# Kernel optimization log

Measured on AMD Instinct MI355X. Metric: run time of the kernel, lower is better.

The kernel has to match this reference:

```python
import jax, jax.numpy as jnp
import numpy as np
from jax import lax

VOCAB = 32000; D = 1024; NL = 4; DI = 2048; S = 16; R = 64; DC = 4
B = 1; L = 1024; EPS = 1e-5


def setup_inputs() -> dict:
    key = jax.random.key(0)
    ks = jax.random.split(key, 16)
    def n(k, shape, s=0.02):
        return jax.random.normal(k, shape, dtype=jnp.float32) * s
    return dict(
        tokens=jax.random.randint(ks[0], (B, L), 0, VOCAB),
        embed=n(ks[1], (VOCAB, D)),
        norm_w=jnp.ones((NL, D), jnp.float32) + n(ks[2], (NL, D)),
        in_proj_w=n(ks[3], (NL, 2 * DI, D)),
        conv_w=n(ks[4], (NL, DI, DC), 0.1),
        conv_b=n(ks[5], (NL, DI)),
        x_proj_w=n(ks[6], (NL, R + 2 * S, DI)),
        dt_proj_w=n(ks[7], (NL, DI, R), 0.1),
        dt_proj_b=n(ks[8], (NL, DI), 0.5),
        A_log=n(ks[9], (NL, DI, S), 0.5),
        D_param=jnp.ones((NL, DI), jnp.float32) + n(ks[10], (NL, DI)),
        out_proj_w=n(ks[11], (NL, D, DI)),
        norm_f_w=jnp.ones((D,), jnp.float32),
        lm_head_w=n(ks[12], (VOCAB, D)),
    )


def _rmsnorm(x, w):
    return x * lax.rsqrt(jnp.mean(x * x, axis=-1, keepdims=True) + EPS) * w


def _mamba_block(x, norm_w, in_w, cw, cb, xw, dtw, dtb, a_log, dp, ow):
    # x: [B, L, D]
    res = x
    x = _rmsnorm(x, norm_w)
    xz = jnp.einsum('bld,ed->ble', x, in_w)      # [B, L, 2*DI]
    u, z = xz[..., :DI], xz[..., DI:]
    # depthwise causal conv over time
    u = jnp.swapaxes(u, 1, 2)                    # [B, DI, L]
    u = lax.conv_general_dilated(u, cw[:, None, :], (1,), [(DC - 1, 0)],
                                 feature_group_count=DI,
                                 dimension_numbers=('NCH', 'OIH', 'NCH'))
    u = jax.nn.silu(u + cb[None, :, None])
    u = jnp.swapaxes(u, 1, 2)                    # [B, L, DI]
    # input-dependent SSM params
    dbc = jnp.einsum('bld,ed->ble', u, xw)       # [B, L, R+2S]
    dt = jax.nn.softplus(jnp.einsum('blr,dr->bld', dbc[..., :R], dtw) + dtb)
    Bm = dbc[..., R:R + S]                       # [B, L, S]
    Cm = dbc[..., R + S:]                        # [B, L, S]
    A = -jnp.exp(a_log)                          # [DI, S]
    dA = jnp.exp(dt[..., None] * A)              # [B, L, DI, S]
    dBu = (dt * u)[..., None] * Bm[:, :, None, :]  # [B, L, DI, S]
    # selective scan over time
    def step(h, inp):
        a_t, b_t, c_t = inp
        h = a_t * h + b_t                        # [B, DI, S]
        y = jnp.einsum('bds,bs->bd', h, c_t)
        return h, y
    h0 = jnp.zeros((x.shape[0], DI, S), x.dtype)
    _, ys = lax.scan(step, h0, (jnp.moveaxis(dA, 1, 0), jnp.moveaxis(dBu, 1, 0), jnp.moveaxis(Cm, 1, 0)))
    y = jnp.moveaxis(ys, 0, 1) + u * dp          # [B, L, DI]
    y = y * jax.nn.silu(z)
    return res + jnp.einsum('bld,od->blo', y, ow)


def reference(tokens, embed, norm_w, in_proj_w, conv_w, conv_b, x_proj_w,
              dt_proj_w, dt_proj_b, A_log, D_param, out_proj_w, norm_f_w, lm_head_w):
    x = embed[tokens]                            # [B, L, D]
    for i in range(NL):
        x = _mamba_block(x, norm_w[i], in_proj_w[i], conv_w[i], conv_b[i],
                         x_proj_w[i], dt_proj_w[i], dt_proj_b[i], A_log[i],
                         D_param[i], out_proj_w[i])
    x = _rmsnorm(x, norm_f_w)
    return jnp.einsum('bld,vd->blv', x, lm_head_w)  # [B, L, VOCAB]
```

## Files before the change

### kernel.cpp

```cpp
#include <hip/hip_runtime.h>
#include <hip/hip_bf16.h>
#include <math.h>


typedef __attribute__((ext_vector_type(8))) short bf16x8;
typedef __attribute__((ext_vector_type(4))) float f32x4;

__device__ __forceinline__ short f2bf(float f) {
  union { float f; unsigned u; } v; v.f = f;
  unsigned u = v.u;
  unsigned r = (u + 0x7FFFu + ((u >> 16) & 1u)) >> 16;
  return (short)r;
}

__device__ __forceinline__ bf16x8 pack8(float4 a, float4 b) {
  bf16x8 r;
  r[0] = f2bf(a.x); r[1] = f2bf(a.y); r[2] = f2bf(a.z); r[3] = f2bf(a.w);
  r[4] = f2bf(b.x); r[5] = f2bf(b.y); r[6] = f2bf(b.z); r[7] = f2bf(b.w);
  return r;
}

__device__ __forceinline__ float softplus_f(float x) {
  return (x > 20.f) ? x : log1pf(__expf(x));
}

__device__ __forceinline__ void gl_lds16(const void* g, void* l) {
  void* gnc = (void*)g;
  __builtin_amdgcn_global_load_lds((__attribute__((address_space(1))) void*)gnc,
                                   (__attribute__((address_space(3))) void*)l, 16, 0, 0);
}

__global__ __launch_bounds__(256) void cvt_all_k(const float* __restrict__ s0, unsigned short* __restrict__ d0, int n0,
                                                 const float* __restrict__ s1, unsigned short* __restrict__ d1, int n1,
                                                 const float* __restrict__ s2, unsigned short* __restrict__ d2, int n2,
                                                 const float* __restrict__ s3, unsigned short* __restrict__ d3, int n3,
                                                 const float* __restrict__ s4, unsigned short* __restrict__ d4, int n4) {
  int stride = gridDim.x * 256;
  int tot = n0 + n1 + n2 + n3 + n4;
  for (int i = blockIdx.x * 256 + threadIdx.x; i < tot; i += stride) {
    const float* s; unsigned short* d; int j = i;
    if (j < n0) { s = s0; d = d0; }
    else { j -= n0; if (j < n1) { s = s1; d = d1; }
      else { j -= n1; if (j < n2) { s = s2; d = d2; }
        else { j -= n2; if (j < n3) { s = s3; d = d3; }
          else { j -= n3; s = s4; d = d4; } } } }
    const float4* p = (const float4*)(s + (size_t)j * 8);
    float4 a = p[0], b = p[1];
    *(bf16x8*)(d + (size_t)j * 8) = pack8(a, b);
  }
}

__global__ __launch_bounds__(256) void embed_rms_k(const int* __restrict__ tok,
                                                   const float* __restrict__ emb,
                                                   const float* __restrict__ w,
                                                   float* __restrict__ x,
                                                   unsigned short* __restrict__ xn16) {
  int l = blockIdx.x;
  int t = tok[l];
  float4 v = ((const float4*)(emb + (size_t)t * 1024))[threadIdx.x];
  ((float4*)(x + (size_t)l * 1024))[threadIdx.x] = v;
  float ss = v.x * v.x + v.y * v.y + v.z * v.z + v.w * v.w;
  ss += __shfl_down(ss, 32); ss += __shfl_down(ss, 16); ss += __shfl_down(ss, 8);
  ss += __shfl_down(ss, 4);  ss += __shfl_down(ss, 2);  ss += __shfl_down(ss, 1);
  __shared__ float wsum[4];
  if ((threadIdx.x & 63) == 0) wsum[threadIdx.x >> 6] = ss;
  __syncthreads();
  float tot = wsum[0] + wsum[1] + wsum[2] + wsum[3];
  float sc = rsqrtf(tot * (1.0f / 1024.0f) + 1e-5f);
  float4 wv = ((const float4*)w)[threadIdx.x];
  ushort4 o;
  o.x = (unsigned short)f2bf(v.x * sc * wv.x);
  o.y = (unsigned short)f2bf(v.y * sc * wv.y);
  o.z = (unsigned short)f2bf(v.z * sc * wv.z);
  o.w = (unsigned short)f2bf(v.w * sc * wv.w);
  *(ushort4*)(xn16 + (size_t)l * 1024 + threadIdx.x * 4) = o;
}

__global__ __launch_bounds__(256) void rmsnorm16_k(const float* __restrict__ x,
                                                   const float* __restrict__ w,
                                                   unsigned short* __restrict__ y) {
  int l = blockIdx.x;
  const float4* xr = (const float4*)(x + (size_t)l * 1024);
  float4 v = xr[threadIdx.x];
  float ss = v.x * v.x + v.y * v.y + v.z * v.z + v.w * v.w;
  ss += __shfl_down(ss, 32); ss += __shfl_down(ss, 16); ss += __shfl_down(ss, 8);
  ss += __shfl_down(ss, 4);  ss += __shfl_down(ss, 2);  ss += __shfl_down(ss, 1);
  __shared__ float wsum[4];
  if ((threadIdx.x & 63) == 0) wsum[threadIdx.x >> 6] = ss;
  __syncthreads();
  float tot = wsum[0] + wsum[1] + wsum[2] + wsum[3];
  float sc = rsqrtf(tot * (1.0f / 1024.0f) + 1e-5f);
  float4 wv = ((const float4*)w)[threadIdx.x];
  ushort4 o;
  o.x = (unsigned short)f2bf(v.x * sc * wv.x);
  o.y = (unsigned short)f2bf(v.y * sc * wv.y);
  o.z = (unsigned short)f2bf(v.z * sc * wv.z);
  o.w = (unsigned short)f2bf(v.w * sc * wv.w);
  *(ushort4*)(y + (size_t)l * 1024 + threadIdx.x * 4) = o;
}

__global__ __launch_bounds__(256) void rmsnorm_k(const float* __restrict__ x,
                                                 const float* __restrict__ w,
                                                 float* __restrict__ y) {
  int l = blockIdx.x;
  const float4* xr = (const float4*)(x + (size_t)l * 1024);
  float4 v = xr[threadIdx.x];
  float ss = v.x * v.x + v.y * v.y + v.z * v.z + v.w * v.w;
  ss += __shfl_down(ss, 32); ss += __shfl_down(ss, 16); ss += __shfl_down(ss, 8);
  ss += __shfl_down(ss, 4);  ss += __shfl_down(ss, 2);  ss += __shfl_down(ss, 1);
  __shared__ float wsum[4];
  if ((threadIdx.x & 63) == 0) wsum[threadIdx.x >> 6] = ss;
  __syncthreads();
  float tot = wsum[0] + wsum[1] + wsum[2] + wsum[3];
  float sc = rsqrtf(tot * (1.0f / 1024.0f) + 1e-5f);
  float4 wv = ((const float4*)w)[threadIdx.x];
  float4 o;
  o.x = v.x * sc * wv.x; o.y = v.y * sc * wv.y;
  o.z = v.z * sc * wv.z; o.w = v.w * sc * wv.w;
  ((float4*)(y + (size_t)l * 1024))[threadIdx.x] = o;
}

__global__ __launch_bounds__(256) void conv_silu_k(const float* __restrict__ xz,
                                                   const float* __restrict__ cw,
                                                   const float* __restrict__ cb,
                                                   float* __restrict__ u,
                                                   unsigned short* __restrict__ u16) {
  int idx = blockIdx.x * 256 + threadIdx.x;
  int d = idx & 2047;
  int l = idx >> 11;
  float acc = cb[d];
#pragma unroll
  for (int j = 0; j < 4; ++j) {
    int ll = l - 3 + j;
    if (ll >= 0) acc = fmaf(xz[(size_t)ll * 4096 + d], cw[d * 4 + j], acc);
  }
  float sig = 1.0f / (1.0f + __expf(-acc));
  float v = acc * sig;
  u[idx] = v;
  if (u16) u16[idx] = (unsigned short)f2bf(v);
}

__global__ __launch_bounds__(256) void gemm16_k(const unsigned short* __restrict__ A, int lda,
                                                const unsigned short* __restrict__ W, int ldw,
                                                const float* __restrict__ addsrc,
                                                const float* __restrict__ spbias,
                                                float* __restrict__ C, int ldc,
                                                unsigned short* __restrict__ C16,
                                                int gx, int N, int K) {
  int total = gridDim.x;
  int lin = blockIdx.x;
  int q = total >> 3, r = total & 7;
  int xcd = lin & 7, idx = lin >> 3;
  int nl = (xcd < r ? xcd * (q + 1) : r * (q + 1) + (xcd - r) * q) + idx;
  const int bm = (nl % gx) << 7;
  const int bn = (nl / gx) << 7;

  const int tid = threadIdx.x;
  const int wid = tid >> 6;
  const int lane = tid & 63;
  const int wm = (wid >> 1) << 6;
  const int wn = (wid & 1) << 6;
  const int fr = lane & 15;
  const int kg = lane >> 4;
  const int srow = lane >> 3;
  const int sch  = lane & 7;
  const int xch  = sch ^ srow;

  __shared__ unsigned short sA[2][8192];
  __shared__ unsigned short sB[2][8192];

  f32x4 acc[4][4];
#pragma unroll
  for (int i = 0; i < 4; ++i)
#pragma unroll
    for (int j = 0; j < 4; ++j) acc[i][j] = (f32x4){0.f, 0.f, 0.f, 0.f};

  auto STAGE = [&](int b, int k0) {
#pragma unroll
    for (int t = 0; t < 4; ++t) {
      int g = (wid << 2) + t;
      int row = (g << 3) + srow;
      const unsigned short* ga = A + (size_t)(bm + row) * lda + k0 + (xch << 3);
      int wrow = bn + row; if (wrow >= N) wrow = N - 1;
      const unsigned short* gw = W + (size_t)wrow * ldw + k0 + (xch << 3);
      gl_lds16(ga, &sA[b][g << 9]);
      gl_lds16(gw, &sB[b][g << 9]);
    }
  };

  auto COMPUTE = [&](int b) {
#pragma unroll
    for (int ks = 0; ks < 2; ++ks) {
      bf16x8 af[4], bw[4];
#pragma unroll
      for (int mi = 0; mi < 4; ++mi) {
        int row = wm + (mi << 4) + fr;
        int xc = ((ks << 2) + kg) ^ (fr & 7);
        af[mi] = *(const bf16x8*)&sA[b][(row << 6) + (xc << 3)];
      }
#pragma unroll
      for (int ni = 0; ni < 4; ++ni) {
        int row = wn + (ni << 4) + fr;
        int xc = ((ks << 2) + kg) ^ (fr & 7);
        bw[ni] = *(const bf16x8*)&sB[b][(row << 6) + (xc << 3)];
      }
#pragma unroll
      for (int mi = 0; mi < 4; ++mi)
#pragma unroll
        for (int ni = 0; ni < 4; ++ni)
          acc[mi][ni] = __builtin_amdgcn_mfma_f32_16x16x32_bf16(af[mi], bw[ni], acc[mi][ni], 0, 0, 0);
    }
  };

  const int nt = K >> 6;
  STAGE(0, 0);
  int cur = 0;
  for (int t = 0; t + 1 < nt; ++t) {
    STAGE(cur ^ 1, (t + 1) << 6);
    asm volatile("s_waitcnt vmcnt(8)" ::: "memory");
    __builtin_amdgcn_s_barrier();
    __builtin_amdgcn_sched_barrier(0);
    COMPUTE(cur);
    __builtin_amdgcn_s_barrier();
    cur ^= 1;
  }
  asm volatile("s_waitcnt vmcnt(0)" ::: "memory");
  __builtin_amdgcn_s_barrier();
  __builtin_amdgcn_sched_barrier(0);
  COMPUTE(cur);

#pragma unroll
  for (int mi = 0; mi < 4; ++mi)
#pragma unroll
    for (int ni = 0; ni < 4; ++ni) {
      int n = bn + wn + (ni << 4) + fr;
      if (n < N) {
#pragma unroll
        for (int i = 0; i < 4; ++i) {
          int m = bm + wm + (mi << 4) + (kg << 2) + i;
          size_t off = (size_t)m * ldc + n;
          float v = acc[mi][ni][i];
          if (addsrc) v += addsrc[off];
          if (spbias) v = softplus_f(v + spbias[n]);
          C[off] = v;
          if (C16) C16[off] = (unsigned short)f2bf(v);
        }
      }
    }
}

__global__ __launch_bounds__(256) void gemm16sk_k(const unsigned short* __restrict__ A, int lda,
                                                  const unsigned short* __restrict__ W, int ldw,
                                                  float* __restrict__ Cp, int ldc,
                                                  int gx, int N, int Kchunk, int Mtot) {
  int total = gridDim.x;
  int lin = blockIdx.x;
  int q = total >> 3, r = total & 7;
  int xcd = lin & 7, idx = lin >> 3;
  int nl = (xcd < r ? xcd * (q + 1) : r * (q + 1) + (xcd - r) * q) + idx;
  const int bm = (nl % gx) << 7;
  const int bn = (nl / gx) << 7;
  const int ksplit = blockIdx.y;
  const int kbase = ksplit * Kchunk;

  const int tid = threadIdx.x;
  const int wid = tid >> 6;
  const int lane = tid & 63;
  const int wm = (wid >> 1) << 6;
  const int wn = (wid & 1) << 6;
  const int fr = lane & 15;
  const int kg = lane >> 4;
  const int srow = lane >> 3;
  const int sch  = lane & 7;
  const int xch  = sch ^ srow;

  __shared__ unsigned short sA[2][8192];
  __shared__ unsigned short sB[2][8192];

  f32x4 acc[4][4];
#pragma unroll
  for (int i = 0; i < 4; ++i)
#pragma unroll
    for (int j = 0; j < 4; ++j) acc[i][j] = (f32x4){0.f, 0.f, 0.f, 0.f};

  auto STAGE = [&](int b, int k0) {
#pragma unroll
    for (int t = 0; t < 4; ++t) {
      int g = (wid << 2) + t;
      int row = (g << 3) + srow;
      const unsigned short* ga = A + (size_t)(bm + row) * lda + k0 + (xch << 3);
      int wrow = bn + row; if (wrow >= N) wrow = N - 1;
      const unsigned short* gw = W + (size_t)wrow * ldw + k0 + (xch << 3);
      gl_lds16(ga, &sA[b][g << 9]);
      gl_lds16(gw, &sB[b][g << 9]);
    }
  };

  auto COMPUTE = [&](int b) {
#pragma unroll
    for (int ks = 0; ks < 2; ++ks) {
      bf16x8 af[4], bw[4];
#pragma unroll
      for (int mi = 0; mi < 4; ++mi) {
        int row = wm + (mi << 4) + fr;
        int xc = ((ks << 2) + kg) ^ (fr & 7);
        af[mi] = *(const bf16x8*)&sA[b][(row << 6) + (xc << 3)];
      }
#pragma unroll
      for (int ni = 0; ni < 4; ++ni) {
        int row = wn + (ni << 4) + fr;
        int xc = ((ks << 2) + kg) ^ (fr & 7);
        bw[ni] = *(const bf16x8*)&sB[b][(row << 6) + (xc << 3)];
      }
#pragma unroll
      for (int mi = 0; mi < 4; ++mi)
#pragma unroll
        for (int ni = 0; ni < 4; ++ni)
          acc[mi][ni] = __builtin_amdgcn_mfma_f32_16x16x32_bf16(af[mi], bw[ni], acc[mi][ni], 0, 0, 0);
    }
  };

  const int nt = Kchunk >> 6;
  STAGE(0, kbase);
  int cur = 0;
  for (int t = 0; t + 1 < nt; ++t) {
    STAGE(cur ^ 1, kbase + ((t + 1) << 6));
    asm volatile("s_waitcnt vmcnt(8)" ::: "memory");
    __builtin_amdgcn_s_barrier();
    __builtin_amdgcn_sched_barrier(0);
    COMPUTE(cur);
    __builtin_amdgcn_s_barrier();
    cur ^= 1;
  }
  asm volatile("s_waitcnt vmcnt(0)" ::: "memory");
  __builtin_amdgcn_s_barrier();
  __builtin_amdgcn_sched_barrier(0);
  COMPUTE(cur);

  float* Cs = Cp + (size_t)ksplit * Mtot * ldc;
#pragma unroll
  for (int mi = 0; mi < 4; ++mi)
#pragma unroll
    for (int ni = 0; ni < 4; ++ni) {
      int n = bn + wn + (ni << 4) + fr;
      if (n < N) {
#pragma unroll
        for (int i = 0; i < 4; ++i) {
          int m = bm + wm + (mi << 4) + (kg << 2) + i;
          Cs[(size_t)m * ldc + n] = acc[mi][ni][i];
        }
      }
    }
}

__global__ __launch_bounds__(256) void reduce_xp_k(const float* __restrict__ Cp,
                                                   float* __restrict__ dbc,
                                                   unsigned short* __restrict__ dbc16) {
  int i = blockIdx.x * 256 + threadIdx.x;
  float v = Cp[i] + Cp[98304 + i] + Cp[2 * 98304 + i] + Cp[3 * 98304 + i];
  dbc[i] = v;
  dbc16[i] = (unsigned short)f2bf(v);
}

__global__ __launch_bounds__(256) void reduce_op_k(const float* __restrict__ Cp,
                                                   float* __restrict__ x) {
  int i = blockIdx.x * 256 + threadIdx.x;
  const float4* p0 = (const float4*)Cp;
  const float4* p1 = (const float4*)(Cp + 1048576);
  const float4* p2 = (const float4*)(Cp + 2097152);
  const float4* p3 = (const float4*)(Cp + 3145728);
  float4 a = p0[i], b = p1[i], c = p2[i], d = p3[i];
  float4 xv = ((float4*)x)[i];
  xv.x += a.x + b.x + c.x + d.x;
  xv.y += a.y + b.y + c.y + d.y;
  xv.z += a.z + b.z + c.z + d.z;
  xv.w += a.w + b.w + c.w + d.w;
  ((float4*)x)[i] = xv;
}

__global__ __launch_bounds__(512, 2) void gemm256_k(const unsigned short* __restrict__ A, int lda,
                                                    const unsigned short* __restrict__ W, int ldw,
                                                    float* __restrict__ C, int ldc,
                                                    int gx, int N, int K) {
  int total = gridDim.x;
  int lin = blockIdx.x;
  int q = total >> 3, r = total & 7;
  int xcd = lin & 7, idx = lin >> 3;
  int nl = (xcd < r ? xcd * (q + 1) : r * (q + 1) + (xcd - r) * q) + idx;
  const int bm = (nl % gx) << 8;
  const int bn = (nl / gx) << 8;

  const int tid = threadIdx.x;
  const int wid = tid >> 6;
  const int lane = tid & 63;
  const int wm = (wid >> 2) << 7;
  const int wn = (wid & 3) << 6;
  const int fr = lane & 15;
  const int kg = lane >> 4;
  const int srow = lane >> 3;
  const int sch  = lane & 7;
  const int xch  = sch ^ srow;

  __shared__ unsigned short sA[2][16384];
  __shared__ unsigned short sB[2][16384];

  f32x4 acc[8][4];
#pragma unroll
  for (int i = 0; i < 8; ++i)
#pragma unroll
    for (int j = 0; j < 4; ++j) acc[i][j] = (f32x4){0.f, 0.f, 0.f, 0.f};

  auto STAGE = [&](int b, int k0) {
#pragma unroll
    for (int t = 0; t < 4; ++t) {
      int g = (wid << 2) + t;
      int row = (g << 3) + srow;
      const unsigned short* ga = A + (size_t)(bm + row) * lda + k0 + (xch << 3);
      int wrow = bn + row; if (wrow >= N) wrow = N - 1;
      const unsigned short* gw = W + (size_t)wrow * ldw + k0 + (xch << 3);
      gl_lds16(ga, &sA[b][g << 9]);
      gl_lds16(gw, &sB[b][g << 9]);
    }
  };

  auto COMPUTE = [&](int b) {
#pragma unroll
    for (int ks = 0; ks < 2; ++ks) {
      bf16x8 af[8], bw[4];
#pragma unroll
      for (int mi = 0; mi < 8; ++mi) {
        int row = wm + (mi << 4) + fr;
        int xc = ((ks << 2) + kg) ^ (fr & 7);
        af[mi] = *(const bf16x8*)&sA[b][(row << 6) + (xc << 3)];
      }
#pragma unroll
      for (int ni = 0; ni < 4; ++ni) {
        int row = wn + (ni << 4) + fr;
        int xc = ((ks << 2) + kg) ^ (fr & 7);
        bw[ni] = *(const bf16x8*)&sB[b][(row << 6) + (xc << 3)];
      }
#pragma unroll
      for (int mi = 0; mi < 8; ++mi)
#pragma unroll
        for (int ni = 0; ni < 4; ++ni)
          acc[mi][ni] = __builtin_amdgcn_mfma_f32_16x16x32_bf16(af[mi], bw[ni], acc[mi][ni], 0, 0, 0);
    }
  };

  const int nt = K >> 6;
  STAGE(0, 0);
  int cur = 0;
  for (int t = 0; t + 1 < nt; ++t) {
    STAGE(cur ^ 1, (t + 1) << 6);
    asm volatile("s_waitcnt vmcnt(8)" ::: "memory");
    __builtin_amdgcn_s_barrier();
    __builtin_amdgcn_sched_barrier(0);
    COMPUTE(cur);
    __builtin_amdgcn_s_barrier();
    cur ^= 1;
  }
  asm volatile("s_waitcnt vmcnt(0)" ::: "memory");
  __builtin_amdgcn_s_barrier();
  __builtin_amdgcn_sched_barrier(0);
  COMPUTE(cur);

#pragma unroll
  for (int mi = 0; mi < 8; ++mi)
#pragma unroll
    for (int ni = 0; ni < 4; ++ni) {
      int n = bn + wn + (ni << 4) + fr;
      if (n < N) {
#pragma unroll
        for (int i = 0; i < 4; ++i) {
          int m = bm + wm + (mi << 4) + (kg << 2) + i;
          C[(size_t)m * ldc + n] = acc[mi][ni][i];
        }
      }
    }
}

__global__ __launch_bounds__(256) void gemm_bt_k(const float* __restrict__ A, int lda,
                                                 const float* __restrict__ W, int ldw,
                                                 const float* __restrict__ addsrc,
                                                 float* __restrict__ C, int ldc,
                                                 int N, int K) {
  const int tid  = threadIdx.x;
  const int srow = tid >> 1;
  const int skg  = (tid & 1) << 1;
  const int bm = blockIdx.x << 7;
  const int bn = blockIdx.y << 7;
  const int wid = tid >> 6;
  const int lane = tid & 63;
  const int wm = (wid >> 1) << 6;
  const int wn = (wid & 1) << 6;
  const int fr = lane & 15;
  const int kg = lane >> 4;

  __shared__ bf16x8 lA[4][128];
  __shared__ bf16x8 lB[4][128];

  f32x4 zero4 = {0.f, 0.f, 0.f, 0.f};
  f32x4 acc[4][4];
#pragma unroll
  for (int i = 0; i < 4; ++i)
#pragma unroll
    for (int j = 0; j < 4; ++j) acc[i][j] = zero4;

  const bool wvalid = (bn + srow) < N;
  const float* gA = A + (size_t)(bm + srow) * lda + (skg << 3);
  const float* gW = W + (size_t)(wvalid ? (bn + srow) : 0) * ldw + (skg << 3);

  for (int k0 = 0; k0 < K; k0 += 32) {
    float4 a0 = *(const float4*)(gA + k0);
    float4 a1 = *(const float4*)(gA + k0 + 4);
    float4 a2 = *(const float4*)(gA + k0 + 8);
    float4 a3 = *(const float4*)(gA + k0 + 12);
    float4 w0 = make_float4(0.f, 0.f, 0.f, 0.f), w1 = w0, w2 = w0, w3 = w0;
    if (wvalid) {
      w0 = *(const float4*)(gW + k0);
      w1 = *(const float4*)(gW + k0 + 4);
      w2 = *(const float4*)(gW + k0 + 8);
      w3 = *(const float4*)(gW + k0 + 12);
    }
    __syncthreads();
    lA[skg][srow]     = pack8(a0, a1);
    lA[skg + 1][srow] = pack8(a2, a3);
    lB[skg][srow]     = pack8(w0, w1);
    lB[skg + 1][srow] = pack8(w2, w3);
    __syncthreads();

    bf16x8 af[4], bf_[4];
#pragma unroll
    for (int mi = 0; mi < 4; ++mi) af[mi] = lA[kg][wm + (mi << 4) + fr];
#pragma unroll
    for (int ni = 0; ni < 4; ++ni) bf_[ni] = lB[kg][wn + (ni << 4) + fr];
#pragma unroll
    for (int mi = 0; mi < 4; ++mi)
#pragma unroll
      for (int ni = 0; ni < 4; ++ni)
        acc[mi][ni] = __builtin_amdgcn_mfma_f32_16x16x32_bf16(af[mi], bf_[ni], acc[mi][ni], 0, 0, 0);
  }

#pragma unroll
  for (int mi = 0; mi < 4; ++mi)
#pragma unroll
    for (int ni = 0; ni < 4; ++ni) {
      int n = bn + wn + (ni << 4) + fr;
      if (n < N) {
#pragma unroll
        for (int i = 0; i < 4; ++i) {
          int m = bm + wm + (mi << 4) + (kg << 2) + i;
          size_t off = (size_t)m * ldc + n;
          float v = acc[mi][ni][i];
          if (addsrc) v += addsrc[off];
          C[off] = v;
        }
      }
    }
}

#define NCH 32
#define CHL 32

__global__ __launch_bounds__(256) void scan_p1f_k(const float* __restrict__ dtv,
                                                  const float* __restrict__ u,
                                                  const float* __restrict__ dbc,
                                                  const float* __restrict__ A_log,
                                                  float* __restrict__ Pg,
                                                  float* __restrict__ qg) {
  int tid = threadIdx.x;
  int s = tid & 15, dg = tid >> 4;
  int d = (blockIdx.x << 4) + dg;
  int c = blockIdx.y;
  int l0 = c << 5;
  float A = -__expf(A_log[d * 16 + s]);
  float P = 1.f, q = 0.f;
#pragma unroll 4
  for (int i = 0; i < CHL; ++i) {
    int l = l0 + i;
    size_t rd = (size_t)l * 2048 + d;
    float dt = dtv[rd];
    float dA = __expf(dt * A);
    P *= dA;
    q = fmaf(dA, q, dt * u[rd] * dbc[l * 96 + 64 + s]);
  }
  size_t o = (size_t)c * 32768 + d * 16 + s;
  Pg[o] = P;
  qg[o] = q;
}

__global__ __launch_bounds__(256) void scan_p3f_k(const float* __restrict__ dtv,
                                                  const float* __restrict__ u,
                                                  const float* __restrict__ dbc,
                                                  const float* __restrict__ xz,
                                                  const float* __restrict__ A_log,
                                                  const float* __restrict__ Dp,
                                                  const float* __restrict__ Pg,
                                                  const float* __restrict__ qg,
                                                  unsigned short* __restrict__ y16) {
  int tid = threadIdx.x;
  int s = tid & 15, dg = tid >> 4;
  int d = (blockIdx.x << 4) + dg;
  int c = blockIdx.y;
  int l0 = c << 5;
  float A = -__expf(A_log[d * 16 + s]);
  float dpar = Dp[d];
  float h = 0.f;
  for (int cc = 0; cc < c; ++cc) {
    size_t o = (size_t)cc * 32768 + d * 16 + s;
    h = fmaf(Pg[o], h, qg[o]);
  }
#pragma unroll 4
  for (int i = 0; i < CHL; ++i) {
    int l = l0 + i;
    size_t rd = (size_t)l * 2048 + d;
    float dt = dtv[rd];
    float uv = u[rd];
    float dA = __expf(dt * A);
    h = fmaf(dA, h, dt * uv * dbc[l * 96 + 64 + s]);
    float p = h * dbc[l * 96 + 80 + s];
    p += __shfl_xor(p, 1); p += __shfl_xor(p, 2);
    p += __shfl_xor(p, 4); p += __shfl_xor(p, 8);
    if (s == 0) {
      float zv = xz[(size_t)l * 4096 + 2048 + d];
      float sig = 1.0f / (1.0f + __expf(-zv));
      y16[rd] = (unsigned short)f2bf((p + uv * dpar) * (zv * sig));
    }
  }
}

__global__ __launch_bounds__(256) void scan_p1_k(const float* __restrict__ dtr,
                                                 const float* __restrict__ u,
                                                 const float* __restrict__ dbc,
                                                 const float* __restrict__ A_log,
                                                 const float* __restrict__ dtb,
                                                 float* __restrict__ Pg,
                                                 float* __restrict__ qg) {
  int tid = threadIdx.x;
  int s = tid & 15, dg = tid >> 4;
  int d = (blockIdx.x << 4) + dg;
  int c = blockIdx.y;
  int l0 = c << 5;
  float A = -__expf(A_log[d * 16 + s]);
  float bias = dtb[d];
  float P = 1.f, q = 0.f;
#pragma unroll 4
  for (int i = 0; i < CHL; ++i) {
    int l = l0 + i;
    float dt = softplus_f(dtr[(size_t)l * 2048 + d] + bias);
    float dA = __expf(dt * A);
    P *= dA;
    q = fmaf(dA, q, dt * u[(size_t)l * 2048 + d] * dbc[l * 96 + 64 + s]);
  }
  size_t o = (size_t)c * 32768 + d * 16 + s;
  Pg[o] = P;
  qg[o] = q;
}

__global__ __launch_bounds__(256) void scan_p2_k(const float* __restrict__ Pg,
                                                 const float* __restrict__ qg,
                                                 float* __restrict__ hst) {
  int idx = blockIdx.x * 256 + threadIdx.x;
  float h = 0.f;
#pragma unroll
  for (int c = 0; c < NCH; ++c) {
    size_t o = (size_t)c * 32768 + idx;
    hst[o] = h;
    h = fmaf(Pg[o], h, qg[o]);
  }
}

__global__ __launch_bounds__(256) void scan_p3_k(const float* __restrict__ dtr,
                                                 const float* __restrict__ u,
                                                 const float* __restrict__ dbc,
                                                 const float* __restrict__ xz,
                                                 const float* __restrict__ A_log,
                                                 const float* __restrict__ Dp,
                                                 const float* __restrict__ dtb,
                                                 const float* __restrict__ hst,
                                                 float* __restrict__ y) {
  int tid = threadIdx.x;
  int s = tid & 15, dg = tid >> 4;
  int d = (blockIdx.x << 4) + dg;
  int c = blockIdx.y;
  int l0 = c << 5;
  float A = -__expf(A_log[d * 16 + s]);
  float dpar = Dp[d];
  float bias = dtb[d];
  float h = hst[(size_t)c * 32768 + d * 16 + s];
#pragma unroll 4
  for (int i = 0; i < CHL; ++i) {
    int l = l0 + i;
    size_t rd = (size_t)l * 2048 + d;
    float dt = softplus_f(dtr[rd] + bias);
    float uv = u[rd];
    float dA = __expf(dt * A);
    h = fmaf(dA, h, dt * uv * dbc[l * 96 + 64 + s]);
    float p = h * dbc[l * 96 + 80 + s];
    p += __shfl_xor(p, 1); p += __shfl_xor(p, 2);
    p += __shfl_xor(p, 4); p += __shfl_xor(p, 8);
    if (s == 0) {
      float zv = xz[(size_t)l * 4096 + 2048 + d];
      float sig = 1.0f / (1.0f + __expf(-zv));
      y[rd] = (p + uv * dpar) * (zv * sig);
    }
  }
}

extern "C" void kernel_launch(void* const* d_in, const int* in_sizes, int n_in,
                              void* d_out, int out_size, void* d_ws, size_t ws_size,
                              hipStream_t stream) {
  const int*   tokens = (const int*)d_in[0];
  const float* embed  = (const float*)d_in[1];
  const float* norm_w = (const float*)d_in[2];
  const float* in_w   = (const float*)d_in[3];
  const float* conv_w = (const float*)d_in[4];
  const float* conv_b = (const float*)d_in[5];
  const float* x_w    = (const float*)d_in[6];
  const float* dt_w   = (const float*)d_in[7];
  const float* dt_b   = (const float*)d_in[8];
  const float* A_log  = (const float*)d_in[9];
  const float* D_par  = (const float*)d_in[10];
  const float* out_w  = (const float*)d_in[11];
  const float* normf  = (const float*)d_in[12];
  const float* lm_w   = (const float*)d_in[13];

  float* out = (float*)d_out;
  float* x    = out;
  float* xz   = x    + 1024 * 1024;
  float* u    = xz   + 1024 * 4096;
  float* dtv  = u    + 1024 * 2048;
  float* dbc  = dtv  + 1024 * 2048;
  float* Pg   = dbc  + 1024 * 96;
  float* qg   = Pg   + 32 * 32768;
  float* hst  = qg   + 32 * 32768;
  float* xn_f = hst  + 32 * 32768;
  float* y_f  = xn_f + 1024 * 1024;
  unsigned short* xn16  = (unsigned short*)(y_f + 1024 * 2048);
  unsigned short* u16   = xn16 + 1024 * 1024;
  unsigned short* y16   = u16  + 1024 * 2048;
  unsigned short* dbc16 = y16  + 1024 * 2048;
  float* part_op = (float*)(dbc16 + 1024 * 96);
  float* part_xp = part_op + 4 * 1048576;

  unsigned short* inw16 = (unsigned short*)d_ws;
  unsigned short* oww16 = inw16 + 16777216;
  unsigned short* xw16  = oww16 + 8388608;
  unsigned short* dtw16 = xw16  + 786432;
  unsigned short* lmw16 = dtw16 + 524288;
  unsigned short* xnf16 = lmw16 + 32768000;
  const size_t need = (size_t)(16777216 + 8388608 + 786432 + 524288 + 32768000 + 1048576) * 2;
  const bool fast = ws_size >= need;

  if (fast) {
    cvt_all_k<<<4096, 256, 0, stream>>>(in_w, inw16, 2097152,
                                        out_w, oww16, 1048576,
                                        x_w, xw16, 98304,
                                        dt_w, dtw16, 65536,
                                        lm_w, lmw16, 4096000);
    embed_rms_k<<<1024, 256, 0, stream>>>(tokens, embed, norm_w, x, xn16);

    for (int i = 0; i < 4; ++i) {
      if (i > 0) rmsnorm16_k<<<1024, 256, 0, stream>>>(x, norm_w + i * 1024, xn16);
      gemm16_k<<<256, 256, 0, stream>>>(xn16, 1024, inw16 + (size_t)i * 4194304, 1024,
                                        nullptr, nullptr, xz, 4096, nullptr, 8, 4096, 1024);
      conv_silu_k<<<8192, 256, 0, stream>>>(xz, conv_w + i * 8192, conv_b + i * 2048, u, u16);
      gemm16sk_k<<<dim3(8, 4), 256, 0, stream>>>(u16, 2048, xw16 + (size_t)i * 196608, 2048,
                                                 part_xp, 96, 8, 96, 512, 1024);
      reduce_xp_k<<<384, 256, 0, stream>>>(part_xp, dbc, dbc16);
      gemm16_k<<<128, 256, 0, stream>>>(dbc16, 96, dtw16 + (size_t)i * 131072, 64,
                                        nullptr, dt_b + i * 2048, dtv, 2048, nullptr, 8, 2048, 64);
      scan_p1f_k<<<dim3(128, NCH), 256, 0, stream>>>(dtv, u, dbc, A_log + i * 32768, Pg, qg);
      scan_p3f_k<<<dim3(128, NCH), 256, 0, stream>>>(dtv, u, dbc, xz, A_log + i * 32768,
                                                     D_par + i * 2048, Pg, qg, y16);
      gemm16sk_k<<<dim3(64, 4), 256, 0, stream>>>(y16, 2048, oww16 + (size_t)i * 2097152, 2048,
                                                  part_op, 1024, 8, 1024, 512, 1024);
      reduce_op_k<<<1024, 256, 0, stream>>>(part_op, x);
    }

    rmsnorm16_k<<<1024, 256, 0, stream>>>(x, normf, xnf16);
    gemm256_k<<<500, 512, 0, stream>>>(xnf16, 1024, lmw16, 1024, out, 32000, 4, 32000, 1024);
  } else {
    float* xnf_f = (float*)d_ws;
    embed_rms_k<<<1024, 256, 0, stream>>>(tokens, embed, norm_w, x, xn16);
    for (int i = 0; i < 4; ++i) {
      rmsnorm_k<<<1024, 256, 0, stream>>>(x, norm_w + i * 1024, xn_f);
      gemm_bt_k<<<dim3(8, 32), 256, 0, stream>>>(xn_f, 1024, in_w + (size_t)i * 4194304, 1024,
                                                 nullptr, xz, 4096, 4096, 1024);
      conv_silu_k<<<8192, 256, 0, stream>>>(xz, conv_w + i * 8192, conv_b + i * 2048, u, nullptr);
      gemm_bt_k<<<dim3(8, 1), 256, 0, stream>>>(u, 2048, x_w + (size_t)i * 196608, 2048,
                                                nullptr, dbc, 96, 96, 2048);
      gemm_bt_k<<<dim3(8, 16), 256, 0, stream>>>(dbc, 96, dt_w + (size_t)i * 131072, 64,
                                                 nullptr, dtv, 2048, 2048, 64);
      scan_p1_k<<<dim3(128, NCH), 256, 0, stream>>>(dtv, u, dbc, A_log + i * 32768,
                                                    dt_b + i * 2048, Pg, qg);
      scan_p2_k<<<128, 256, 0, stream>>>(Pg, qg, hst);
      scan_p3_k<<<dim3(128, NCH), 256, 0, stream>>>(dtv, u, dbc, xz, A_log + i * 32768,
                                                    D_par + i * 2048, dt_b + i * 2048, hst, y_f);
      gemm_bt_k<<<dim3(8, 8), 256, 0, stream>>>(y_f, 2048, out_w + (size_t)i * 2097152, 2048,
                                                x, x, 1024, 1024, 2048);
    }
    rmsnorm_k<<<1024, 256, 0, stream>>>(x, normf, xnf_f);
    gemm_bt_k<<<dim3(8, 250), 256, 0, stream>>>(xnf_f, 1024, lm_w, 1024,
                                                nullptr, out, 32000, 32000, 1024);
  }
}
```

Before: 946.0 us.

## Fuse lm_head fp32-to-bf16 conversion into the vocab GEMM's B-tile staging

The lm_head weight is no longer pre-converted to bf16 in a separate pass. The vocab GEMM now loads fp32 weight rows into registers, converts them with packed bf16 conversion, and writes them into swizzled LDS, pipelined across two buffers. This removes a 131MB read plus 65MB write conversion pass, but doubles the GEMM's weight read bytes and adds register pressure, since launch bounds lose the 2-blocks hint. The remaining weight conversion kernel is restructured per block and uses a hardware pack instruction.

Result: slower. 1.037 ms (+9.6%).

```diff
diff --git a/kernel.cpp b/kernel.cpp
--- a/kernel.cpp
+++ b/kernel.cpp
@@ -20,6 +20,12 @@
   return r;
 }
 
+__device__ __forceinline__ unsigned cvtpk(float lo, float hi) {
+  unsigned r;
+  asm("v_cvt_pk_bf16_f32 %0, %1, %2" : "=v"(r) : "v"(lo), "v"(hi));
+  return r;
+}
+
 __device__ __forceinline__ float softplus_f(float x) {
   return (x > 20.f) ? x : log1pf(__expf(x));
 }
@@ -30,23 +36,26 @@
                                    (__attribute__((address_space(3))) void*)l, 16, 0, 0);
 }
 
-__global__ __launch_bounds__(256) void cvt_all_k(const float* __restrict__ s0, unsigned short* __restrict__ d0, int n0,
-                                                 const float* __restrict__ s1, unsigned short* __restrict__ d1, int n1,
-                                                 const float* __restrict__ s2, unsigned short* __restrict__ d2, int n2,
-                                                 const float* __restrict__ s3, unsigned short* __restrict__ d3, int n3,
-                                                 const float* __restrict__ s4, unsigned short* __restrict__ d4, int n4) {
-  int stride = gridDim.x * 256;
-  int tot = n0 + n1 + n2 + n3 + n4;
-  for (int i = blockIdx.x * 256 + threadIdx.x; i < tot; i += stride) {
-    const float* s; unsigned short* d; int j = i;
-    if (j < n0) { s = s0; d = d0; }
-    else { j -= n0; if (j < n1) { s = s1; d = d1; }
-      else { j -= n1; if (j < n2) { s = s2; d = d2; }
-        else { j -= n2; if (j < n3) { s = s3; d = d3; }
-          else { j -= n3; s = s4; d = d4; } } } }
-    const float4* p = (const float4*)(s + (size_t)j * 8);
-    float4 a = p[0], b = p[1];
-    *(bf16x8*)(d + (size_t)j * 8) = pack8(a, b);
+__global__ __launch_bounds__(256) void cvt4_k(const float* __restrict__ s0, unsigned short* __restrict__ d0, int nb0,
+                                              const float* __restrict__ s1, unsigned short* __restrict__ d1, int nb1,
+                                              const float* __restrict__ s2, unsigned short* __restrict__ d2, int nb2,
+                                              const float* __restrict__ s3, unsigned short* __restrict__ d3, int nb3) {
+  int b = blockIdx.x;
+  const float* s; unsigned short* d; int lb;
+  if (b < nb0) { s = s0; d = d0; lb = b; }
+  else if (b < nb0 + nb1) { s = s1; d = d1; lb = b - nb0; }
+  else if (b < nb0 + nb1 + nb2) { s = s2; d = d2; lb = b - nb0 - nb1; }
+  else { s = s3; d = d3; lb = b - nb0 - nb1 - nb2; }
+  size_t base = (size_t)lb * 1024;
+#pragma unroll
+  for (int u = 0; u < 4; ++u) {
+    size_t idx = base + u * 256 + threadIdx.x;
+    const float4* p = (const float4*)(s + idx * 8);
+    float4 a = p[0], bq = p[1];
+    uint4 w;
+    w.x = cvtpk(a.x, a.y); w.y = cvtpk(a.z, a.w);
+    w.z = cvtpk(bq.x, bq.y); w.w = cvtpk(bq.z, bq.w);
+    *(uint4*)(d + idx * 8) = w;
   }
 }
 
@@ -378,10 +387,12 @@
   ((float4*)x)[i] = xv;
 }
 
-__global__ __launch_bounds__(512, 2) void gemm256_k(const unsigned short* __restrict__ A, int lda,
-                                                    const unsigned short* __restrict__ W, int ldw,
-                                                    float* __restrict__ C, int ldc,
-                                                    int gx, int N, int K) {
+struct WREG { float4 v[8]; };
+
+__global__ __launch_bounds__(512) void gemm256f_k(const unsigned short* __restrict__ A, int lda,
+                                                  const float* __restrict__ W, int ldw,
+                                                  float* __restrict__ C, int ldc,
+                                                  int gx, int N, int K) {
   int total = gridDim.x;
   int lin = blockIdx.x;
   int q = total >> 3, r = total & 7;
@@ -401,6 +412,11 @@
   const int sch  = lane & 7;
   const int xch  = sch ^ srow;
 
+  const int wr_row  = tid >> 1;
+  const int wr_half = tid & 1;
+  int wr_grow = bn + wr_row; if (wr_grow >= N) wr_grow = N - 1;
+  const float* gWrow = W + (size_t)wr_grow * ldw + wr_half * 32;
+
   __shared__ unsigned short sA[2][16384];
   __shared__ unsigned short sB[2][16384];
 
@@ -410,20 +426,36 @@
 #pragma unroll
     for (int j = 0; j < 4; ++j) acc[i][j] = (f32x4){0.f, 0.f, 0.f, 0.f};
 
-  auto STAGE = [&](int b, int k0) {
+  auto STAGE_A = [&](unsigned short* buf, int k0) {
 #pragma unroll
     for (int t = 0; t < 4; ++t) {
       int g = (wid << 2) + t;
       int row = (g << 3) + srow;
       const unsigned short* ga = A + (size_t)(bm + row) * lda + k0 + (xch << 3);
-      int wrow = bn + row; if (wrow >= N) wrow = N - 1;
-      const unsigned short* gw = W + (size_t)wrow * ldw + k0 + (xch << 3);
-      gl_lds16(ga, &sA[b][g << 9]);
-      gl_lds16(gw, &sB[b][g << 9]);
+      gl_lds16(ga, &buf[g << 9]);
     }
   };
 
-  auto COMPUTE = [&](int b) {
+  auto WLOAD = [&](WREG& w, int k0) {
+    const float4* p = (const float4*)(gWrow + k0);
+#pragma unroll
+    for (int j = 0; j < 8; ++j) w.v[j] = p[j];
+  };
+
+  auto WWRITE = [&](unsigned short* buf, const WREG& w) {
+#pragma unroll
+    for (int c2 = 0; c2 < 4; ++c2) {
+      int c = (wr_half << 2) + c2;
+      uint4 val;
+      val.x = cvtpk(w.v[2 * c2].x,     w.v[2 * c2].y);
+      val.y = cvtpk(w.v[2 * c2].z,     w.v[2 * c2].w);
+      val.z = cvtpk(w.v[2 * c2 + 1].x, w.v[2 * c2 + 1].y);
+      val.w = cvtpk(w.v[2 * c2 + 1].z, w.v[2 * c2 + 1].w);
+      *(uint4*)&buf[(wr_row << 6) + ((c ^ (wr_row & 7)) << 3)] = val;
+    }
+  };
+
+  auto COMPUTE = [&](const unsigned short* bufa, const unsigned short* bufb) {
 #pragma unroll
     for (int ks = 0; ks < 2; ++ks) {
       bf16x8 af[8], bw[4];
@@ -431,13 +463,13 @@
       for (int mi = 0; mi < 8; ++mi) {
         int row = wm + (mi << 4) + fr;
         int xc = ((ks << 2) + kg) ^ (fr & 7);
-        af[mi] = *(const bf16x8*)&sA[b][(row << 6) + (xc << 3)];
+        af[mi] = *(const bf16x8*)&bufa[(row << 6) + (xc << 3)];
       }
 #pragma unroll
       for (int ni = 0; ni < 4; ++ni) {
         int row = wn + (ni << 4) + fr;
         int xc = ((ks << 2) + kg) ^ (fr & 7);
-        bw[ni] = *(const bf16x8*)&sB[b][(row << 6) + (xc << 3)];
+        bw[ni] = *(const bf16x8*)&bufb[(row << 6) + (xc << 3)];
       }
 #pragma unroll
       for (int mi = 0; mi < 8; ++mi)
@@ -448,21 +480,55 @@
   };
 
   const int nt = K >> 6;
-  STAGE(0, 0);
-  int cur = 0;
-  for (int t = 0; t + 1 < nt; ++t) {
-    STAGE(cur ^ 1, (t + 1) << 6);
-    asm volatile("s_waitcnt vmcnt(8)" ::: "memory");
+  WREG wrA, wrB;
+
+  STAGE_A(sA[0], 0);
+  WLOAD(wrA, 0);
+  STAGE_A(sA[1], 64);
+  WLOAD(wrB, 64);
+  __builtin_amdgcn_sched_barrier(0);
+  asm volatile("s_waitcnt vmcnt(12)" ::: "memory");
+  __builtin_amdgcn_sched_barrier(0);
+  WWRITE(sB[0], wrA);
+  asm volatile("s_waitcnt lgkmcnt(0)" ::: "memory");
+  __builtin_amdgcn_s_barrier();
+  __builtin_amdgcn_sched_barrier(0);
+
+  for (int tt = 0; tt < nt; tt += 2) {
+    COMPUTE(sA[0], sB[0]);
+    __builtin_amdgcn_s_barrier();
+    if (tt + 2 < nt) {
+      STAGE_A(sA[0], (tt + 2) << 6);
+      WLOAD(wrA, (tt + 2) << 6);
+      __builtin_amdgcn_sched_barrier(0);
+      asm volatile("s_waitcnt vmcnt(12)" ::: "memory");
+    } else {
+      asm volatile("s_waitcnt vmcnt(0)" ::: "memory");
+    }
+    __builtin_amdgcn_sched_barrier(0);
+    WWRITE(sB[1], wrB);
+    asm volatile("s_waitcnt lgkmcnt(0)" ::: "memory");
     __builtin_amdgcn_s_barrier();
     __builtin_amdgcn_sched_barrier(0);
-    COMPUTE(cur);
-    __builtin_amdgcn_s_barrier();
-    cur ^= 1;
-  }
-  asm volatile("s_waitcnt vmcnt(0)" ::: "memory");
-  __builtin_amdgcn_s_barrier();
-  __builtin_amdgcn_sched_barrier(0);
-  COMPUTE(cur);
+
+    COMPUTE(sA[1], sB[1]);
+    if (tt + 2 < nt) {
+      __builtin_amdgcn_s_barrier();
+      if (tt + 3 < nt) {
+        STAGE_A(sA[1], (tt + 3) << 6);
+        WLOAD(wrB, (tt + 3) << 6);
+        __builtin_amdgcn_sched_barrier(0);
+        asm volatile("s_waitcnt vmcnt(12)" ::: "memory");
+      } else {
+        asm volatile("s_waitcnt vmcnt(0)" ::: "memory");
+      }
+      __builtin_amdgcn_sched_barrier(0);
+      WWRITE(sB[0], wrA);
+      asm volatile("s_waitcnt lgkmcnt(0)" ::: "memory");
+      __builtin_amdgcn_s_barrier();
+      __builtin_amdgcn_sched_barrier(0);
+    }
+  }
 
 #pragma unroll
   for (int mi = 0; mi < 8; ++mi)
@@ -747,17 +813,15 @@
   unsigned short* oww16 = inw16 + 16777216;
   unsigned short* xw16  = oww16 + 8388608;
   unsigned short* dtw16 = xw16  + 786432;
-  unsigned short* lmw16 = dtw16 + 524288;
-  unsigned short* xnf16 = lmw16 + 32768000;
-  const size_t need = (size_t)(16777216 + 8388608 + 786432 + 524288 + 32768000 + 1048576) * 2;
+  unsigned short* xnf16 = dtw16 + 524288;
+  const size_t need = (size_t)(16777216 + 8388608 + 786432 + 524288 + 1048576) * 2;
   const bool fast = ws_size >= need;
 
   if (fast) {
-    cvt_all_k<<<4096, 256, 0, stream>>>(in_w, inw16, 2097152,
-                                        out_w, oww16, 1048576,
-                                        x_w, xw16, 98304,
-                                        dt_w, dtw16, 65536,
-                                        lm_w, lmw16, 4096000);
+    cvt4_k<<<3232, 256, 0, stream>>>(in_w, inw16, 2048,
+                                     out_w, oww16, 1024,
+                                     x_w, xw16, 96,
+                                     dt_w, dtw16, 64);
     embed_rms_k<<<1024, 256, 0, stream>>>(tokens, embed, norm_w, x, xn16);
 
     for (int i = 0; i < 4; ++i) {
@@ -779,7 +843,7 @@
     }
 
     rmsnorm16_k<<<1024, 256, 0, stream>>>(x, normf, xnf16);
-    gemm256_k<<<500, 512, 0, stream>>>(xnf16, 1024, lmw16, 1024, out, 32000, 4, 32000, 1024);
+    gemm256f_k<<<500, 512, 0, stream>>>(xnf16, 1024, lm_w, 1024, out, 32000, 4, 32000, 1024);
   } else {
     float* xnf_f = (float*)d_ws;
     embed_rms_k<<<1024, 256, 0, stream>>>(tokens, embed, norm_w, x, xn16);
```
